# Optimization experiments

Measured on AMD Instinct MI355X. Metric: run time of the kernel, lower is better.

Reference implementation:

```python
import jax, jax.numpy as jnp
import numpy as np

N = 50000
E = 1600000
IN_CH = 128
HID = 32
HEADS = 4
NEG_SLOPE = 0.2
BN_EPS = 1e-5


def _gat_layer(x, src, dst, W, att_src, att_dst, n):
    """PyG-style GATConv (no bias; bias added by caller).
    x: [n, f_in], W: [f_in, heads*out], att_*: [heads, out].
    Returns [n, heads, out]."""
    heads, out_ch = att_src.shape
    h = (x @ W).reshape(n, heads, out_ch)                 # node projections
    a_s = jnp.einsum('nhc,hc->nh', h, att_src)            # per-node src logit
    a_d = jnp.einsum('nhc,hc->nh', h, att_dst)            # per-node dst logit
    e = jax.nn.leaky_relu(a_s[src] + a_d[dst], NEG_SLOPE)  # [E_tot, heads]
    m = jax.ops.segment_max(e, dst, num_segments=n)       # per-target max (stable softmax)
    ex = jnp.exp(e - m[dst])
    denom = jax.ops.segment_sum(ex, dst, num_segments=n)
    alpha = ex / denom[dst]                               # segment softmax over incoming edges
    out = jax.ops.segment_sum(h[src] * alpha[:, :, None], dst, num_segments=n)
    return out


def setup_inputs():
    key = jax.random.key(0)
    ks = jax.random.split(key, 8)
    x = jax.random.normal(ks[0], (N, IN_CH), dtype=jnp.float32)
    edge_index = jax.random.randint(ks[1], (2, E), 0, N, dtype=jnp.int32)
    s1 = 1.0 / float(np.sqrt(IN_CH))
    W1 = jax.random.uniform(ks[2], (IN_CH, HEADS * HID), jnp.float32, -s1, s1)
    att_src1 = jax.random.uniform(ks[3], (HEADS, HID), jnp.float32, -s1, s1)
    att_dst1 = jax.random.uniform(ks[4], (HEADS, HID), jnp.float32, -s1, s1)
    bias1 = jnp.zeros((HEADS * HID,), jnp.float32)
    bn_gamma = jnp.ones((HEADS * HID,), jnp.float32)
    bn_beta = jnp.zeros((HEADS * HID,), jnp.float32)
    bn_mean = jnp.zeros((HEADS * HID,), jnp.float32)
    bn_var = jnp.ones((HEADS * HID,), jnp.float32)
    s2 = 1.0 / float(np.sqrt(HEADS * HID))
    W2 = jax.random.uniform(ks[5], (HEADS * HID, 2), jnp.float32, -s2, s2)
    att_src2 = jax.random.uniform(ks[6], (1, 2), jnp.float32, -s2, s2)
    att_dst2 = jax.random.uniform(ks[7], (1, 2), jnp.float32, -s2, s2)
    bias2 = jnp.zeros((2,), jnp.float32)
    return {"x": x, "edge_index": edge_index, "W1": W1, "att_src1": att_src1,
            "att_dst1": att_dst1, "bias1": bias1, "bn_gamma": bn_gamma,
            "bn_beta": bn_beta, "bn_mean": bn_mean, "bn_var": bn_var,
            "W2": W2, "att_src2": att_src2, "att_dst2": att_dst2, "bias2": bias2}


def reference(x, edge_index, W1, att_src1, att_dst1, bias1, bn_gamma, bn_beta,
              bn_mean, bn_var, W2, att_src2, att_dst2, bias2):
    n = x.shape[0]
    # PyG GATConv default add_self_loops=True
    loop = jnp.arange(n, dtype=edge_index.dtype)
    src = jnp.concatenate([edge_index[0], loop])
    dst = jnp.concatenate([edge_index[1], loop])
    # conv1 (concat=True) + bias
    h1 = _gat_layer(x, src, dst, W1, att_src1, att_dst1, n).reshape(n, -1) + bias1
    # BatchNorm1d (eval mode, running stats)
    h1 = bn_gamma * (h1 - bn_mean) / jnp.sqrt(bn_var + BN_EPS) + bn_beta
    h1 = jax.nn.leaky_relu(h1, NEG_SLOPE)
    # dropout is identity in eval mode
    # conv2 (heads=1, concat=False -> mean over heads) + bias
    h2 = _gat_layer(h1, src, dst, W2, att_src2, att_dst2, n).mean(axis=1) + bias2
    return jax.nn.log_softmax(h2, axis=1)
```

## Files before the change

### kernel.cpp

```cpp
#include <hip/hip_runtime.h>
#include <math.h>

#define NN 50000
#define EE 1600000
#define FIN 128
#define FOUT 128
#define NEG 0.2f
#define BNEPS 1e-5f

#define NPART 8
#define PSZ (NN / NPART)

#define BEB 1024
#define NBUCK ((EE + BEB - 1) / BEB)
#define GGRP 8
#define BCAPG 30000
#define DSUB 8

static __device__ __forceinline__ unsigned f2bf(float f) {
  unsigned int u = __float_as_uint(f);
  u += 0x7fffu + ((u >> 16) & 1u);
  return u >> 16;
}

#define XSS 66
__global__ __launch_bounds__(256) void k_proj(const float* __restrict__ x,
    const float* __restrict__ W1, const float* __restrict__ asw, const float* __restrict__ adw,
    signed char* __restrict__ h8, float* __restrict__ hscale,
    float* __restrict__ as1, float* __restrict__ ad1) {
  __shared__ unsigned xs[64 * XSS];
  int t = threadIdx.x;
  int nb = blockIdx.x * 64;

  #pragma unroll
  for (int j = 0; j < 8; ++j) {
    int idx = t + 256 * j;
    int r = idx >> 5;
    int c4 = idx & 31;
    int n = nb + r; if (n >= NN) n = NN - 1;
    float4 v = *(const float4*)(x + (size_t)n * FIN + c4 * 4);
    xs[r * XSS + c4 * 2]     = f2bf(v.x) | (f2bf(v.y) << 16);
    xs[r * XSS + c4 * 2 + 1] = f2bf(v.z) | (f2bf(v.w) << 16);
  }
  __syncthreads();

  int cg = t & 15;
  int ng = t >> 4;
  int c0 = cg * 8;

  float acc[4][8];
  #pragma unroll
  for (int i = 0; i < 4; ++i)
    #pragma unroll
    for (int j = 0; j < 8; ++j) acc[i][j] = 0.f;

  for (int k0 = 0; k0 < FIN; k0 += 4) {
    float xr[4][4];
    #pragma unroll
    for (int i = 0; i < 4; ++i) {
      uint2 u = *(const uint2*)&xs[(ng * 4 + i) * XSS + (k0 >> 1)];
      xr[i][0] = __uint_as_float(u.x << 16);
      xr[i][1] = __uint_as_float(u.x & 0xffff0000u);
      xr[i][2] = __uint_as_float(u.y << 16);
      xr[i][3] = __uint_as_float(u.y & 0xffff0000u);
    }
    #pragma unroll
    for (int kk = 0; kk < 4; ++kk) {
      float4 w0 = *(const float4*)(W1 + (k0 + kk) * FOUT + c0);
      float4 w1 = *(const float4*)(W1 + (k0 + kk) * FOUT + c0 + 4);
      float wv[8] = {w0.x, w0.y, w0.z, w0.w, w1.x, w1.y, w1.z, w1.w};
      #pragma unroll
      for (int i = 0; i < 4; ++i) {
        float xv = xr[i][kk];
        #pragma unroll
        for (int j = 0; j < 8; ++j) acc[i][j] = fmaf(xv, wv[j], acc[i][j]);
      }
    }
  }

  int head = cg >> 2;
  float vs[4], vd[4], rmax[4];
  #pragma unroll
  for (int i = 0; i < 4; ++i) {
    float s = 0.f, d = 0.f, m = 0.f;
    #pragma unroll
    for (int j = 0; j < 8; ++j) {
      s = fmaf(acc[i][j], asw[c0 + j], s);
      d = fmaf(acc[i][j], adw[c0 + j], d);
      m = fmaxf(m, fabsf(acc[i][j]));
    }
    vs[i] = s; vd[i] = d; rmax[i] = m;
  }
  #pragma unroll
  for (int i = 0; i < 4; ++i) {
    rmax[i] = fmaxf(rmax[i], __shfl_xor(rmax[i], 1, 64));
    rmax[i] = fmaxf(rmax[i], __shfl_xor(rmax[i], 2, 64));
    rmax[i] = fmaxf(rmax[i], __shfl_xor(rmax[i], 4, 64));
    rmax[i] = fmaxf(rmax[i], __shfl_xor(rmax[i], 8, 64));
  }
  #pragma unroll
  for (int i = 0; i < 4; ++i) {
    int n = nb + ng * 4 + i;
    if (n >= NN) continue;
    float rm = fmaxf(rmax[i], 1e-30f);
    float inv = 127.f / rm;
    unsigned b[8];
    #pragma unroll
    for (int j = 0; j < 8; ++j) {
      float qf = fminf(127.f, fmaxf(-127.f, rintf(acc[i][j] * inv)));
      b[j] = (unsigned)((int)qf) & 0xffu;
    }
    uint2 pk;
    pk.x = b[0] | (b[1] << 8) | (b[2] << 16) | (b[3] << 24);
    pk.y = b[4] | (b[5] << 8) | (b[6] << 16) | (b[7] << 24);
    *(uint2*)(h8 + (size_t)n * FOUT + c0) = pk;
    if (cg == 0) hscale[n] = rm / 127.f;
  }
  #pragma unroll
  for (int i = 0; i < 4; ++i) {
    vs[i] += __shfl_xor(vs[i], 1, 64); vs[i] += __shfl_xor(vs[i], 2, 64);
    vd[i] += __shfl_xor(vd[i], 1, 64); vd[i] += __shfl_xor(vd[i], 2, 64);
  }
  if ((cg & 3) == 0) {
    #pragma unroll
    for (int i = 0; i < 4; ++i) {
      int n = nb + ng * 4 + i;
      if (n < NN) { as1[n * 4 + head] = vs[i]; ad1[n * 4 + head] = vd[i]; }
    }
  }
}

__global__ __launch_bounds__(256) void k_bucket(const int* __restrict__ ei,
    int* __restrict__ bcur, unsigned* __restrict__ bkt) {
  __shared__ int lcnt[NPART];
  __shared__ int gbase[NPART];
  int t = threadIdx.x;
  int g = blockIdx.x & (GGRP - 1);
  if (t < NPART) lcnt[t] = 0;
  __syncthreads();
  int e0 = blockIdx.x * BEB;
  int part[4]; int lslot[4]; unsigned pk[4];
  #pragma unroll
  for (int j = 0; j < 4; ++j) {
    int i = e0 + j * 256 + t;
    if (i < EE) {
      int s = ei[i];
      int d = ei[EE + i];
      int p = d / PSZ;
      part[j] = p;
      pk[j] = (unsigned)s | ((unsigned)(d - p * PSZ) << 17);
      lslot[j] = atomicAdd(&lcnt[p], 1);
    } else part[j] = -1;
  }
  __syncthreads();
  if (t < NPART) gbase[t] = atomicAdd(&bcur[(g * NPART + t) * 16], lcnt[t]);
  __syncthreads();
  #pragma unroll
  for (int j = 0; j < 4; ++j) {
    if (part[j] >= 0)
      bkt[(size_t)(g * NPART + part[j]) * BCAPG + gbase[part[j]] + lslot[j]] = pk[j];
  }
}

__global__ __launch_bounds__(1024) void k_deg(const int* __restrict__ bcur,
    const unsigned* __restrict__ bkt, int* __restrict__ degp) {
  __shared__ int lh[PSZ];
  int t = threadIdx.x;
  int part = blockIdx.x & (NPART - 1);
  int g    = blockIdx.x >> 3;
  for (int i = t; i < PSZ; i += 1024) lh[i] = 0;
  __syncthreads();
  int cnt = bcur[(g * NPART + part) * 16];
  const unsigned* b = bkt + (size_t)(g * NPART + part) * BCAPG;
  for (int i = t; i < cnt; i += 1024)
    atomicAdd(&lh[b[i] >> 17], 1);
  __syncthreads();
  int* dst = degp + ((size_t)part * DSUB + g) * PSZ;
  for (int i = t; i < PSZ; i += 1024) dst[i] = lh[i];
}

__global__ __launch_bounds__(1024) void k_scat4(const int* __restrict__ bcur,
    const unsigned* __restrict__ bkt, const int* __restrict__ degp,
    int* __restrict__ offs, int* __restrict__ csr) {
  __shared__ int lcur[PSZ];
  __shared__ int sums[1024];
  __shared__ int sb[GGRP * NPART];
  int t = threadIdx.x;
  int p = blockIdx.x & (NPART - 1);
  int g = blockIdx.x >> 3;
  if (t < GGRP * NPART) sb[t] = bcur[t * 16];
  __syncthreads();

  int base_p = 0;
  for (int pp = 0; pp < p; ++pp) {
    int s = PSZ;
    for (int gg = 0; gg < GGRP; ++gg) s += sb[gg * NPART + pp];
    base_p += s;
  }

  const int CH = 7;
  int n0 = t * CH;
  int tsum = 0;
  for (int i = 0; i < CH; ++i) {
    int idx = n0 + i;
    if (idx < PSZ) {
      int v = 1;
      for (int gg = 0; gg < GGRP; ++gg)
        v += degp[((size_t)p * DSUB + gg) * PSZ + idx];
      tsum += v;
    }
  }
  sums[t] = tsum; __syncthreads();
  for (int off = 1; off < 1024; off <<= 1) {
    int u = (t >= off) ? sums[t - off] : 0;
    __syncthreads();
    sums[t] += u;
    __syncthreads();
  }
  int run = base_p + ((t == 0) ? 0 : sums[t - 1]);
  for (int i = 0; i < CH; ++i) {
    int idx = n0 + i;
    if (idx < PSZ) {
      int v = 1, pre = 0;
      for (int gg = 0; gg < GGRP; ++gg) {
        int d = degp[((size_t)p * DSUB + gg) * PSZ + idx];
        v += d;
        if (gg < g) pre += d;
      }
      if (g == 0) offs[p * PSZ + idx] = run;
      lcur[idx] = run + pre;
      run += v;
    }
  }
  if (g == 0 && p == NPART - 1 && t == 1023)
    offs[NN] = base_p + sums[1023];
  __syncthreads();

  int cnt = sb[g * NPART + p];
  const unsigned* b = bkt + (size_t)(g * NPART + p) * BCAPG;
  for (int i = t; i < cnt; i += 1024) {
    unsigned v = b[i];
    int pos = atomicAdd(&lcur[v >> 17], 1);
    csr[pos] = (int)(v & 0x1ffffu);
  }
  if (g == DSUB - 1) {
    __syncthreads();
    for (int i = t; i < PSZ; i += 1024)
      csr[lcur[i]] = p * PSZ + i;
  }
}

__global__ __launch_bounds__(256) void k_agg1(
    const int* __restrict__ offs, const int* __restrict__ csr,
    const signed char* __restrict__ h8, const float* __restrict__ hscale,
    const float* __restrict__ as1, const float* __restrict__ ad1,
    const float* __restrict__ bias1, const float* __restrict__ gamma, const float* __restrict__ beta,
    const float* __restrict__ mean, const float* __restrict__ var,
    const float* __restrict__ W2, const float* __restrict__ asw2, const float* __restrict__ adw2,
    float* __restrict__ h2, float* __restrict__ as2, float* __restrict__ ad2) {
  __shared__ uint2 swlds[4][32][4];
  int wid = threadIdx.x >> 6;
  int lane = threadIdx.x & 63;
  int n = blockIdx.x * 4 + wid;
  if (n >= NN) return;
  int r0 = offs[n], r1 = offs[n + 1];
  int l  = lane & 31;
  int hf = lane >> 5;
  int hh = l >> 3;
  const signed char* hpb = h8;
  float2 adv = *(const float2*)(ad1 + n * 4 + hf * 2);

  float acc0 = 0.f, acc1 = 0.f, acc2 = 0.f, acc3 = 0.f;
  float denp0 = 0.f, denp1 = 0.f;

#define AGG_PRE(IDX, PRED)                                         \
  {                                                                \
    int sv = csr[(IDX)];                                           \
    float hs = hscale[sv];                                         \
    float2 av = *(const float2*)(as1 + sv * 4 + hf * 2);           \
    float e0 = av.x + adv.x; e0 = e0 > 0.f ? e0 : NEG * e0;        \
    float e1 = av.y + adv.y; e1 = e1 > 0.f ? e1 : NEG * e1;        \
    float ex0 = __expf(e0), ex1 = __expf(e1);                      \
    if (PRED) { denp0 += ex0; denp1 += ex1; }                      \
    float w0 = (PRED) ? ex0 * hs : 0.f;                            \
    float w1 = (PRED) ? ex1 * hs : 0.f;                            \
    swlds[wid][l][hf * 2]     = make_uint2((unsigned)sv, __float_as_uint(w0)); \
    swlds[wid][l][hf * 2 + 1] = make_uint2((unsigned)sv, __float_as_uint(w1)); \
  }

#define AGG_BODY(J)                                                \
  {                                                                \
    uint2 sw = swlds[wid][hf * 16 + (J)][hh];                      \
    int s = (int)sw.x;                                             \
    float w = __uint_as_float(sw.y);                               \
    unsigned pv = *(const unsigned*)(hpb + (size_t)s * FOUT + l * 4); \
    int q0 = ((int)(pv << 24)) >> 24;                              \
    int q1 = ((int)(pv << 16)) >> 24;                              \
    int q2 = ((int)(pv << 8)) >> 24;                               \
    int q3 = ((int)pv) >> 24;                                      \
    acc0 = fmaf(w, (float)q0, acc0);                               \
    acc1 = fmaf(w, (float)q1, acc1);                               \
    acc2 = fmaf(w, (float)q2, acc2);                               \
    acc3 = fmaf(w, (float)q3, acc3);                               \
  }

  int base = r0;
  for (; base + 32 <= r1; base += 32) {
    AGG_PRE(base + l, true)
    #pragma unroll
    for (int j = 0; j < 16; ++j) AGG_BODY(j)
  }
  int m = r1 - base;
  if (m > 0) {
    AGG_PRE(base + (l < m ? l : m - 1), l < m)
    int jmax = m < 16 ? m : 16;
    for (int j = 0; j < jmax; ++j) AGG_BODY(j)
  }

  acc0 += __shfl_xor(acc0, 32, 64);
  acc1 += __shfl_xor(acc1, 32, 64);
  acc2 += __shfl_xor(acc2, 32, 64);
  acc3 += __shfl_xor(acc3, 32, 64);

  #pragma unroll
  for (int mm = 16; mm >= 1; mm >>= 1) {
    denp0 += __shfl_xor(denp0, mm, 64);
    denp1 += __shfl_xor(denp1, mm, 64);
  }
  float dOA = __shfl_xor(denp0, 32, 64);
  float dOB = __shfl_xor(denp1, 32, 64);
  float den0 = hf ? dOA : denp0;
  float den1 = hf ? dOB : denp1;
  float den2 = hf ? denp0 : dOA;
  float den3 = hf ? denp1 : dOB;
  float den = (hh == 0) ? den0 : (hh == 1) ? den1 : (hh == 2) ? den2 : den3;

  int c0 = l * 4;
  float inv = 1.f / den;
  float4 bi = *(const float4*)(bias1 + c0);
  float4 ga = *(const float4*)(gamma + c0);
  float4 be = *(const float4*)(beta + c0);
  float4 mu = *(const float4*)(mean + c0);
  float4 va = *(const float4*)(var + c0);
  float o0 = acc0 * inv + bi.x;
  float o1 = acc1 * inv + bi.y;
  float o2 = acc2 * inv + bi.z;
  float o3 = acc3 * inv + bi.w;
  o0 = ga.x * (o0 - mu.x) * rsqrtf(va.x + BNEPS) + be.x;
  o1 = ga.y * (o1 - mu.y) * rsqrtf(va.y + BNEPS) + be.y;
  o2 = ga.z * (o2 - mu.z) * rsqrtf(va.z + BNEPS) + be.z;
  o3 = ga.w * (o3 - mu.w) * rsqrtf(va.w + BNEPS) + be.w;
  o0 = o0 > 0.f ? o0 : NEG * o0;
  o1 = o1 > 0.f ? o1 : NEG * o1;
  o2 = o2 > 0.f ? o2 : NEG * o2;
  o3 = o3 > 0.f ? o3 : NEG * o3;

  float p0 = o0 * W2[(c0 + 0) * 2 + 0] + o1 * W2[(c0 + 1) * 2 + 0]
           + o2 * W2[(c0 + 2) * 2 + 0] + o3 * W2[(c0 + 3) * 2 + 0];
  float p1 = o0 * W2[(c0 + 0) * 2 + 1] + o1 * W2[(c0 + 1) * 2 + 1]
           + o2 * W2[(c0 + 2) * 2 + 1] + o3 * W2[(c0 + 3) * 2 + 1];
  #pragma unroll
  for (int mm = 16; mm >= 1; mm >>= 1) {
    p0 += __shfl_xor(p0, mm, 64);
    p1 += __shfl_xor(p1, mm, 64);
  }
  if (lane == 0) {
    h2[n * 2 + 0] = p0;
    h2[n * 2 + 1] = p1;
    as2[n] = p0 * asw2[0] + p1 * asw2[1];
    ad2[n] = p0 * adw2[0] + p1 * adw2[1];
  }
}

__global__ __launch_bounds__(256) void k_agg2(
    const int* __restrict__ offs, const int* __restrict__ csr,
    const float* __restrict__ h2, const float* __restrict__ as2, const float* __restrict__ ad2,
    const float* __restrict__ bias2, float* __restrict__ out) {
  int wid = threadIdx.x >> 6;
  int lane = threadIdx.x & 63;
  int n = blockIdx.x * 4 + wid;
  if (n >= NN) return;
  int r0 = offs[n], r1 = offs[n + 1];
  float ad = ad2[n];

  float den = 0.f, a0 = 0.f, a1 = 0.f;
  for (int i = r0 + lane; i < r1; i += 64) {
    int s = csr[i];
    float e = as2[s] + ad; e = e > 0.f ? e : NEG * e;
    float ex = __expf(e);
    float2 hv = *(const float2*)(h2 + s * 2);
    den += ex;
    a0 = fmaf(ex, hv.x, a0);
    a1 = fmaf(ex, hv.y, a1);
  }
  #pragma unroll
  for (int mm = 32; mm >= 1; mm >>= 1) {
    den += __shfl_xor(den, mm, 64);
    a0  += __shfl_xor(a0, mm, 64);
    a1  += __shfl_xor(a1, mm, 64);
  }
  if (lane == 0) {
    float o0 = a0 / den + bias2[0];
    float o1 = a1 / den + bias2[1];
    float mx = fmaxf(o0, o1);
    float lse = mx + logf(__expf(o0 - mx) + __expf(o1 - mx));
    out[n * 2 + 0] = o0 - lse;
    out[n * 2 + 1] = o1 - lse;
  }
}

extern "C" void kernel_launch(void* const* d_in, const int* in_sizes, int n_in,
                              void* d_out, int out_size, void* d_ws, size_t ws_size,
                              hipStream_t stream) {
  const float* x     = (const float*)d_in[0];
  const int*   ei    = (const int*)d_in[1];
  const float* W1    = (const float*)d_in[2];
  const float* asw1  = (const float*)d_in[3];
  const float* adw1  = (const float*)d_in[4];
  const float* bias1 = (const float*)d_in[5];
  const float* gamma = (const float*)d_in[6];
  const float* beta  = (const float*)d_in[7];
  const float* mean  = (const float*)d_in[8];
  const float* var   = (const float*)d_in[9];
  const float* W2    = (const float*)d_in[10];
  const float* asw2  = (const float*)d_in[11];
  const float* adw2  = (const float*)d_in[12];
  const float* bias2 = (const float*)d_in[13];
  float* out = (float*)d_out;

  char* ws = (char*)d_ws;
  size_t off = 0;
  auto alloc = [&](size_t bytes) {
    void* p = ws + off;
    off += (bytes + 255) & ~(size_t)255;
    return p;
  };
  signed char* h8 = (signed char*)alloc((size_t)NN * FOUT);
  float* hscale = (float*)alloc((size_t)NN * 4);
  float* as1  = (float*)alloc((size_t)NN * 4 * 4);
  float* ad1  = (float*)alloc((size_t)NN * 4 * 4);
  int*   degp = (int*)alloc((size_t)NPART * DSUB * PSZ * 4);
  int*   offs = (int*)alloc(((size_t)NN + 1) * 4);
  int*   bcur = (int*)alloc((size_t)GGRP * NPART * 16 * 4);
  int*   csr  = (int*)alloc((size_t)(EE + NN) * 4);
  unsigned* bkt = (unsigned*)alloc((size_t)GGRP * NPART * BCAPG * 4);
  float* h2   = (float*)alloc((size_t)NN * 2 * 4);
  float* as2  = (float*)alloc((size_t)NN * 4);
  float* ad2  = (float*)alloc((size_t)NN * 4);
  (void)ws_size; (void)in_sizes; (void)n_in; (void)out_size;

  hipMemsetAsync(bcur, 0, (size_t)GGRP * NPART * 16 * 4, stream);
  k_proj   <<<(NN + 63) / 64, 256, 0, stream>>>(x, W1, asw1, adw1, h8, hscale, as1, ad1);
  k_bucket <<<NBUCK, 256, 0, stream>>>(ei, bcur, bkt);
  k_deg    <<<NPART * DSUB, 1024, 0, stream>>>(bcur, bkt, degp);
  k_scat4  <<<NPART * DSUB, 1024, 0, stream>>>(bcur, bkt, degp, offs, csr);
  k_agg1   <<<(NN + 3) / 4, 256, 0, stream>>>(offs, csr, h8, hscale, as1, ad1, bias1, gamma, beta,
                                              mean, var, W2, asw2, adw2, h2, as2, ad2);
  k_agg2   <<<(NN + 3) / 4, 256, 0, stream>>>(offs, csr, h2, as2, ad2, bias2, out);
}
```

Measured before the change: 193.1 us.

## Fold bucket-counter reset into projection, keep fp32 x tile, split agg LDS

Removes the separate hipMemsetAsync by having block 0 of the projection kernel zero the bucket counters, saving one launch on the stream. The projection kernel now keeps x as fp32 in shared memory instead of converting to bf16, which doubles LDS use but drops the conversion and unpacking ALU work. The first aggregation kernel stores source offsets (premultiplied by row width) and weights in separate LDS arrays, reducing per-edge LDS traffic and address arithmetic. The larger fp32 tile may lower occupancy in the projection kernel.

New measurement: 165.7 us, median of 3. 14.2% less time.

```diff
diff --git a/kernel.cpp b/kernel.cpp
--- a/kernel.cpp
+++ b/kernel.cpp
@@ -17,20 +17,18 @@
 #define BCAPG 30000
 #define DSUB 8
 
-static __device__ __forceinline__ unsigned f2bf(float f) {
-  unsigned int u = __float_as_uint(f);
-  u += 0x7fffu + ((u >> 16) & 1u);
-  return u >> 16;
-}
-
-#define XSS 66
+#define XS_STRIDE 132
 __global__ __launch_bounds__(256) void k_proj(const float* __restrict__ x,
     const float* __restrict__ W1, const float* __restrict__ asw, const float* __restrict__ adw,
     signed char* __restrict__ h8, float* __restrict__ hscale,
-    float* __restrict__ as1, float* __restrict__ ad1) {
-  __shared__ unsigned xs[64 * XSS];
+    float* __restrict__ as1, float* __restrict__ ad1, int* __restrict__ bcur) {
+  __shared__ float xs[64 * XS_STRIDE];
   int t = threadIdx.x;
   int nb = blockIdx.x * 64;
+
+  if (blockIdx.x == 0) {
+    for (int i = t; i < GGRP * NPART * 16; i += 256) bcur[i] = 0;
+  }
 
   #pragma unroll
   for (int j = 0; j < 8; ++j) {
@@ -39,8 +37,7 @@
     int c4 = idx & 31;
     int n = nb + r; if (n >= NN) n = NN - 1;
     float4 v = *(const float4*)(x + (size_t)n * FIN + c4 * 4);
-    xs[r * XSS + c4 * 2]     = f2bf(v.x) | (f2bf(v.y) << 16);
-    xs[r * XSS + c4 * 2 + 1] = f2bf(v.z) | (f2bf(v.w) << 16);
+    *(float4*)(&xs[r * XS_STRIDE + c4 * 4]) = v;
   }
   __syncthreads();
 
@@ -57,13 +54,8 @@
   for (int k0 = 0; k0 < FIN; k0 += 4) {
     float xr[4][4];
     #pragma unroll
-    for (int i = 0; i < 4; ++i) {
-      uint2 u = *(const uint2*)&xs[(ng * 4 + i) * XSS + (k0 >> 1)];
-      xr[i][0] = __uint_as_float(u.x << 16);
-      xr[i][1] = __uint_as_float(u.x & 0xffff0000u);
-      xr[i][2] = __uint_as_float(u.y << 16);
-      xr[i][3] = __uint_as_float(u.y & 0xffff0000u);
-    }
+    for (int i = 0; i < 4; ++i)
+      *(float4*)xr[i] = *(const float4*)&xs[(ng * 4 + i) * XS_STRIDE + k0];
     #pragma unroll
     for (int kk = 0; kk < 4; ++kk) {
       float4 w0 = *(const float4*)(W1 + (k0 + kk) * FOUT + c0);
@@ -258,7 +250,8 @@
     const float* __restrict__ mean, const float* __restrict__ var,
     const float* __restrict__ W2, const float* __restrict__ asw2, const float* __restrict__ adw2,
     float* __restrict__ h2, float* __restrict__ as2, float* __restrict__ ad2) {
-  __shared__ uint2 swlds[4][32][4];
+  __shared__ int   slds[4][32];
+  __shared__ float wlds[4][32][4];
   int wid = threadIdx.x >> 6;
   int lane = threadIdx.x & 63;
   int n = blockIdx.x * 4 + wid;
@@ -267,6 +260,7 @@
   int l  = lane & 31;
   int hf = lane >> 5;
   int hh = l >> 3;
+  int l4 = l * 4;
   const signed char* hpb = h8;
   float2 adv = *(const float2*)(ad1 + n * 4 + hf * 2);
 
@@ -281,19 +275,18 @@
     float e0 = av.x + adv.x; e0 = e0 > 0.f ? e0 : NEG * e0;        \
     float e1 = av.y + adv.y; e1 = e1 > 0.f ? e1 : NEG * e1;        \
     float ex0 = __expf(e0), ex1 = __expf(e1);                      \
+    float w0 = ex0 * hs, w1 = ex1 * hs;                            \
     if (PRED) { denp0 += ex0; denp1 += ex1; }                      \
-    float w0 = (PRED) ? ex0 * hs : 0.f;                            \
-    float w1 = (PRED) ? ex1 * hs : 0.f;                            \
-    swlds[wid][l][hf * 2]     = make_uint2((unsigned)sv, __float_as_uint(w0)); \
-    swlds[wid][l][hf * 2 + 1] = make_uint2((unsigned)sv, __float_as_uint(w1)); \
+    wlds[wid][l][hf * 2]     = (PRED) ? w0 : 0.f;                  \
+    wlds[wid][l][hf * 2 + 1] = (PRED) ? w1 : 0.f;                  \
+    if (hf == 0) slds[wid][l] = sv * FOUT;                         \
   }
 
 #define AGG_BODY(J)                                                \
   {                                                                \
-    uint2 sw = swlds[wid][hf * 16 + (J)][hh];                      \
-    int s = (int)sw.x;                                             \
-    float w = __uint_as_float(sw.y);                               \
-    unsigned pv = *(const unsigned*)(hpb + (size_t)s * FOUT + l * 4); \
+    int soff = slds[wid][hf * 16 + (J)];                           \
+    float w = wlds[wid][hf * 16 + (J)][hh];                        \
+    unsigned pv = *(const unsigned*)(hpb + soff + l4);             \
     int q0 = ((int)(pv << 24)) >> 24;                              \
     int q1 = ((int)(pv << 16)) >> 24;                              \
     int q2 = ((int)(pv << 8)) >> 24;                               \
@@ -449,8 +442,7 @@
   float* ad2  = (float*)alloc((size_t)NN * 4);
   (void)ws_size; (void)in_sizes; (void)n_in; (void)out_size;
 
-  hipMemsetAsync(bcur, 0, (size_t)GGRP * NPART * 16 * 4, stream);
-  k_proj   <<<(NN + 63) / 64, 256, 0, stream>>>(x, W1, asw1, adw1, h8, hscale, as1, ad1);
+  k_proj   <<<(NN + 63) / 64, 256, 0, stream>>>(x, W1, asw1, adw1, h8, hscale, as1, ad1, bcur);
   k_bucket <<<NBUCK, 256, 0, stream>>>(ei, bcur, bkt);
   k_deg    <<<NPART * DSUB, 1024, 0, stream>>>(bcur, bkt, degp);
   k_scat4  <<<NPART * DSUB, 1024, 0, stream>>>(bcur, bkt, degp, offs, csr);
```
